# Kernel tuning notes

Hardware: AMD Instinct MI355X
Metric: run time of the kernel (lower is better)

Reference implementation:

```python
import jax, jax.numpy as jnp
import numpy as np

D_MODEL = 1024
D_K = 1024
D_V = 1024
THRESH = 0.9
LN_EPS = 1e-6


def setup_inputs() -> dict:
    key = jax.random.key(0)
    ks = jax.random.split(key, 8)
    B, S = 8, 2048
    scale = 1.0 / np.sqrt(D_MODEL)
    return {
        "q": jax.random.normal(ks[0], (B, S, D_MODEL), dtype=jnp.float32),
        "k": jax.random.normal(ks[1], (B, S, D_MODEL), dtype=jnp.float32),
        "v": jax.random.normal(ks[2], (B, S, D_MODEL), dtype=jnp.float32),
        "Wq": jax.random.normal(ks[3], (D_MODEL, D_K), dtype=jnp.float32) * scale,
        "Wk": jax.random.normal(ks[4], (D_MODEL, D_K), dtype=jnp.float32) * scale,
        "Wv": jax.random.normal(ks[5], (D_MODEL, D_V), dtype=jnp.float32) * scale,
        "Wfc": jax.random.normal(ks[6], (D_V, D_MODEL), dtype=jnp.float32) * (1.0 / np.sqrt(D_V)),
        "ln_gamma": jnp.ones((D_MODEL,), dtype=jnp.float32),
        "ln_beta": jnp.zeros((D_MODEL,), dtype=jnp.float32),
    }


def reference(q, k, v, Wq, Wk, Wv, Wfc, ln_gamma, ln_beta):
    residual = q
    qh = q @ Wq          # [B,S,d_k]
    kh = k @ Wk          # [B,S,d_k]
    vh = v @ Wv          # [B,S,d_v]
    inv_sqrt_dk = jnp.asarray(1.0 / np.sqrt(D_K), dtype=qh.dtype)
    attn = jnp.einsum('bqd,bkd->bqk', qh, kh) * inv_sqrt_dk  # [B,S,S]
    # hard sparsity threshold applied BEFORE softmax (faithful to original)
    attn = jnp.where(attn < THRESH, jnp.asarray(0.0, attn.dtype), attn)
    attn = jax.nn.softmax(attn, axis=-1)
    # dropout is identity in eval mode
    out = jnp.einsum('bqk,bkd->bqd', attn, vh) @ Wfc  # [B,S,d_model]
    out = out + residual
    mean = jnp.mean(out, axis=-1, keepdims=True)
    var = jnp.mean(jnp.square(out - mean), axis=-1, keepdims=True)
    out = (out - mean) * jax.lax.rsqrt(var + LN_EPS) * ln_gamma + ln_beta
    return (out, attn)
```

## Files before the change

kernel.cpp:

```cpp
#include <hip/hip_runtime.h>
#include <hip/hip_bf16.h>
#include <stdint.h>

typedef __attribute__((ext_vector_type(8))) short bf16x8;
typedef __attribute__((ext_vector_type(4))) float f32x4;
typedef __attribute__((ext_vector_type(4))) unsigned short us4;
typedef __attribute__((ext_vector_type(8))) unsigned short us8;

__device__ __forceinline__ unsigned short f2bf(float f) {
  union { float f; unsigned int u; } v; v.f = f;
  unsigned int u = v.u;
  return (unsigned short)((u + 0x7FFFu + ((u >> 16) & 1u)) >> 16);
}
__device__ __forceinline__ float bf2f(unsigned short h) {
  union { unsigned int u; float f; } v; v.u = ((unsigned int)h) << 16;
  return v.f;
}

__device__ __forceinline__ void gload16(const unsigned short* g, unsigned short* l) {
  __builtin_amdgcn_global_load_lds(
      (const __attribute__((address_space(1))) unsigned int*)g,
      (__attribute__((address_space(3))) unsigned int*)l, 16, 0, 0);
}

template <int EPI>
__global__ __launch_bounds__(512, 2)
void gemm2p(const unsigned short* __restrict__ Ap, const unsigned short* __restrict__ Btp,
            void* __restrict__ Cp, float* __restrict__ extra,
            int M, int N, int K, int nbm, int nbn,
            long long sA, long long sB, long long sC)
{
  __shared__ unsigned short ls[65536];
  __shared__ float srow[256][4];

  const int tid = threadIdx.x;
  const int lane = tid & 63;
  const int wid = tid >> 6;
  const int bb = blockIdx.y;
  const int bm = blockIdx.x % nbm, bn = blockIdx.x / nbm;
  const int row0 = bm * 256, col0 = bn * 256;

  const unsigned short* Ab = Ap + (long long)bb * sA;
  const unsigned short* Bb = Btp + (long long)bb * sB;

  const int srw = tid >> 3;
  const int ssl = (tid & 7) ^ ((tid >> 3) & 7);
  const unsigned short* Asrc = Ab + (long long)(row0 + srw) * K + ssl * 8;
  const unsigned short* Bsrc = Bb + (long long)(col0 + srw) * K + ssl * 8;

#define STAGE(KT, BUF) do { \
    unsigned short* _la = ls + (BUF) * 32768 + wid * 512; \
    unsigned short* _lb = _la + 16384; \
    const long long _ko = (long long)(KT) * 64; \
    gload16(Asrc + _ko,             _la); \
    gload16(Asrc + 64ll * K + _ko,  _la + 4096); \
    gload16(Asrc + 128ll * K + _ko, _la + 8192); \
    gload16(Asrc + 192ll * K + _ko, _la + 12288); \
    gload16(Bsrc + _ko,             _lb); \
    gload16(Bsrc + 64ll * K + _ko,  _lb + 4096); \
    gload16(Bsrc + 128ll * K + _ko, _lb + 8192); \
    gload16(Bsrc + 192ll * K + _ko, _lb + 12288); \
  } while (0)

  const int arow = (wid >> 2) * 128 + (lane & 15);
  const int bcol = (wid & 3) * 64 + (lane & 15);
  const int sl0 = ((lane >> 4) ^ (lane & 7)) * 8;
  const int sl1 = ((4 + (lane >> 4)) ^ (lane & 7)) * 8;

  f32x4 acc[8][4];
#pragma unroll
  for (int m = 0; m < 8; ++m)
#pragma unroll
    for (int n = 0; n < 4; ++n) {
      f32x4 z = {0.f, 0.f, 0.f, 0.f};
      acc[m][n] = z;
    }

  STAGE(0, 0);
  const int NT = K >> 6;
  for (int t = 0; t < NT; ++t) {
    const int cb = (t & 1) * 32768;
    asm volatile("s_waitcnt vmcnt(0)" ::: "memory");
    __builtin_amdgcn_s_barrier();
    __builtin_amdgcn_sched_barrier(0);
    if (t + 1 < NT) STAGE(t + 1, (t & 1) ^ 1);
    const unsigned short* As = ls + cb;
    const unsigned short* Bs = ls + cb + 16384;
    bf16x8 af[8], bfr[4];
#pragma unroll
    for (int mf = 0; mf < 8; ++mf)
      af[mf] = *(const bf16x8*)&As[(arow + mf * 16) * 64 + sl0];
#pragma unroll
    for (int nf = 0; nf < 4; ++nf)
      bfr[nf] = *(const bf16x8*)&Bs[(bcol + nf * 16) * 64 + sl0];
    __builtin_amdgcn_s_setprio(1);
#pragma unroll
    for (int mf = 0; mf < 8; ++mf)
#pragma unroll
      for (int nf = 0; nf < 4; ++nf)
        acc[mf][nf] = __builtin_amdgcn_mfma_f32_16x16x32_bf16(af[mf], bfr[nf], acc[mf][nf], 0, 0, 0);
    __builtin_amdgcn_s_setprio(0);
#pragma unroll
    for (int mf = 0; mf < 8; ++mf)
      af[mf] = *(const bf16x8*)&As[(arow + mf * 16) * 64 + sl1];
#pragma unroll
    for (int nf = 0; nf < 4; ++nf)
      bfr[nf] = *(const bf16x8*)&Bs[(bcol + nf * 16) * 64 + sl1];
    __builtin_amdgcn_s_setprio(1);
#pragma unroll
    for (int mf = 0; mf < 8; ++mf)
#pragma unroll
      for (int nf = 0; nf < 4; ++nf)
        acc[mf][nf] = __builtin_amdgcn_mfma_f32_16x16x32_bf16(af[mf], bfr[nf], acc[mf][nf], 0, 0, 0);
    __builtin_amdgcn_s_setprio(0);
  }
#undef STAGE

  if (EPI == 0 || EPI == 3) {
    unsigned short* C = (unsigned short*)Cp + (long long)bb * sC;
    const float* inv = (EPI == 3) ? (extra + (long long)bb * 2048) : nullptr;
#pragma unroll
    for (int mf = 0; mf < 8; ++mf)
#pragma unroll
      for (int nf = 0; nf < 4; ++nf)
#pragma unroll
        for (int i = 0; i < 4; ++i) {
          int gr = row0 + (wid >> 2) * 128 + mf * 16 + (lane >> 4) * 4 + i;
          int gc = col0 + (wid & 3) * 64 + nf * 16 + (lane & 15);
          float x = acc[mf][nf][i];
          if (EPI == 3) x *= inv[gr];
          C[(long long)gr * N + gc] = f2bf(x);
        }
  } else if (EPI == 2) {
    unsigned short* C = (unsigned short*)Cp;
#pragma unroll
    for (int mf = 0; mf < 8; ++mf)
#pragma unroll
      for (int nf = 0; nf < 4; ++nf) {
        int gr = row0 + (wid >> 2) * 128 + mf * 16 + (lane >> 4) * 4;
        int gc = col0 + (wid & 3) * 64 + nf * 16 + (lane & 15);
        int bb2 = gr >> 11, grb = gr & 2047;
        us4 o;
        o[0] = f2bf(acc[mf][nf][0]); o[1] = f2bf(acc[mf][nf][1]);
        o[2] = f2bf(acc[mf][nf][2]); o[3] = f2bf(acc[mf][nf][3]);
        *(us4*)&C[(long long)bb2 * sC + (long long)gc * 2048 + grb] = o;
      }
  } else {
    unsigned short* C = (unsigned short*)Cp + (long long)bb * sC;
    float rs[8][4];
#pragma unroll
    for (int mf = 0; mf < 8; ++mf)
#pragma unroll
      for (int i = 0; i < 4; ++i) rs[mf][i] = 0.f;
#pragma unroll
    for (int mf = 0; mf < 8; ++mf)
#pragma unroll
      for (int nf = 0; nf < 4; ++nf)
#pragma unroll
        for (int i = 0; i < 4; ++i) {
          int gr = row0 + (wid >> 2) * 128 + mf * 16 + (lane >> 4) * 4 + i;
          int gc = col0 + (wid & 3) * 64 + nf * 16 + (lane & 15);
          float s = acc[mf][nf][i] * 0.03125f;
          s = (s < 0.9f) ? 0.f : s;
          float e = __expf(s);
          C[(long long)gr * N + gc] = f2bf(e);
          rs[mf][i] += e;
        }
#pragma unroll
    for (int mf = 0; mf < 8; ++mf)
#pragma unroll
      for (int i = 0; i < 4; ++i) {
        float vv = rs[mf][i];
        vv += __shfl_xor(vv, 1); vv += __shfl_xor(vv, 2);
        vv += __shfl_xor(vv, 4); vv += __shfl_xor(vv, 8);
        if ((lane & 15) == 0)
          srow[(wid >> 2) * 128 + mf * 16 + (lane >> 4) * 4 + i][wid & 3] = vv;
      }
    __syncthreads();
    if (tid < 256) {
      int gr = row0 + tid;
      extra[((long long)bb * M + gr) * nbn + bn] =
          srow[tid][0] + srow[tid][1] + srow[tid][2] + srow[tid][3];
    }
  }
}

__global__ __launch_bounds__(256)
void cvt3(const float* __restrict__ a, const float* __restrict__ b,
          const float* __restrict__ c, unsigned short* __restrict__ oa,
          unsigned short* __restrict__ ob, unsigned short* __restrict__ oc) {
  const long long i = ((long long)blockIdx.x * 256 + threadIdx.x) * 8;
#pragma unroll
  for (int p = 0; p < 3; ++p) {
    const float* src = (p == 0) ? a : (p == 1) ? b : c;
    unsigned short* dst = (p == 0) ? oa : (p == 1) ? ob : oc;
    f32x4 x0 = *(const f32x4*)(src + i);
    f32x4 x1 = *(const f32x4*)(src + i + 4);
    us8 o;
    o[0] = f2bf(x0[0]); o[1] = f2bf(x0[1]); o[2] = f2bf(x0[2]); o[3] = f2bf(x0[3]);
    o[4] = f2bf(x1[0]); o[5] = f2bf(x1[1]); o[6] = f2bf(x1[2]); o[7] = f2bf(x1[3]);
    *(us8*)(dst + i) = o;
  }
}

__global__ __launch_bounds__(256)
void wtrans4(const float* __restrict__ W0, const float* __restrict__ W1,
             const float* __restrict__ W2, const float* __restrict__ W3,
             unsigned short* __restrict__ T0, unsigned short* __restrict__ T1,
             unsigned short* __restrict__ T2, unsigned short* __restrict__ T3) {
  __shared__ float t[32][33];
  const int z = blockIdx.z;
  const float* W = (z == 0) ? W0 : (z == 1) ? W1 : (z == 2) ? W2 : W3;
  unsigned short* WT = (z == 0) ? T0 : (z == 1) ? T1 : (z == 2) ? T2 : T3;
  const int bi = blockIdx.x, bj = blockIdx.y;
  const int c = threadIdx.x & 31;
  const int r0 = threadIdx.x >> 5;
#pragma unroll
  for (int j = 0; j < 4; ++j) {
    int r = r0 + j * 8;
    t[r][c] = W[(long long)(bi * 32 + r) * 1024 + bj * 32 + c];
  }
  __syncthreads();
#pragma unroll
  for (int j = 0; j < 4; ++j) {
    int r = r0 + j * 8;
    WT[(long long)(bj * 32 + r) * 1024 + bi * 32 + c] = f2bf(t[c][r]);
  }
}

__global__ __launch_bounds__(256)
void attn_norm(const unsigned short* __restrict__ e, const float* __restrict__ partials,
               float* __restrict__ attn, float* __restrict__ inv_dens) {
  const long long row = blockIdx.x;
  const int tid = threadIdx.x;
  __shared__ float sden;
  if (tid < 64) {
    float v = (tid < 8) ? partials[row * 8 + tid] : 0.f;
    v += __shfl_xor(v, 1); v += __shfl_xor(v, 2); v += __shfl_xor(v, 4);
    if (tid == 0) sden = v;
  }
  __syncthreads();
  const float inv = 1.0f / sden;
  if (tid == 0) inv_dens[row] = inv;
  us8 x = *(const us8*)(e + row * 2048 + tid * 8);
  f32x4 y0, y1;
#pragma unroll
  for (int i = 0; i < 4; ++i) { y0[i] = bf2f(x[i]) * inv; y1[i] = bf2f(x[i + 4]) * inv; }
  *(f32x4*)(attn + row * 2048 + tid * 8) = y0;
  *(f32x4*)(attn + row * 2048 + tid * 8 + 4) = y1;
}

template <bool QB16>
__global__ __launch_bounds__(256)
void ln_kernel(const unsigned short* __restrict__ fc, const void* __restrict__ qres,
               const float* __restrict__ gamma, const float* __restrict__ beta,
               float* __restrict__ out) {
  const long long row = blockIdx.x;
  const int tid = threadIdx.x;
  __shared__ float sb1[4], sb2[4];
  us4 hv = *(const us4*)(fc + row * 1024 + tid * 4);
  float q0, q1, q2, q3;
  if (QB16) {
    us4 qv = *(const us4*)((const unsigned short*)qres + row * 1024 + tid * 4);
    q0 = bf2f(qv[0]); q1 = bf2f(qv[1]); q2 = bf2f(qv[2]); q3 = bf2f(qv[3]);
  } else {
    f32x4 qv = *(const f32x4*)((const float*)qres + row * 1024 + tid * 4);
    q0 = qv[0]; q1 = qv[1]; q2 = qv[2]; q3 = qv[3];
  }
  float x0 = bf2f(hv[0]) + q0;
  float x1 = bf2f(hv[1]) + q1;
  float x2 = bf2f(hv[2]) + q2;
  float x3 = bf2f(hv[3]) + q3;
  float s = x0 + x1 + x2 + x3;
#pragma unroll
  for (int m = 1; m < 64; m <<= 1) s += __shfl_xor(s, m);
  if ((tid & 63) == 0) sb1[tid >> 6] = s;
  __syncthreads();
  const float mean = (sb1[0] + sb1[1] + sb1[2] + sb1[3]) * (1.0f / 1024.0f);
  float d0 = x0 - mean, d1 = x1 - mean, d2 = x2 - mean, d3 = x3 - mean;
  float vs = d0 * d0 + d1 * d1 + d2 * d2 + d3 * d3;
#pragma unroll
  for (int m = 1; m < 64; m <<= 1) vs += __shfl_xor(vs, m);
  if ((tid & 63) == 0) sb2[tid >> 6] = vs;
  __syncthreads();
  const float var = (sb2[0] + sb2[1] + sb2[2] + sb2[3]) * (1.0f / 1024.0f);
  const float r = rsqrtf(var + 1e-6f);
  f32x4 g = *(const f32x4*)(gamma + tid * 4);
  f32x4 bt = *(const f32x4*)(beta + tid * 4);
  f32x4 o;
  o[0] = d0 * r * g[0] + bt[0];
  o[1] = d1 * r * g[1] + bt[1];
  o[2] = d2 * r * g[2] + bt[2];
  o[3] = d3 * r * g[3] + bt[3];
  *(f32x4*)(out + row * 1024 + tid * 4) = o;
}

extern "C" void kernel_launch(void* const* d_in, const int* in_sizes, int n_in,
                              void* d_out, int out_size, void* d_ws, size_t ws_size,
                              hipStream_t stream) {
  const float* q    = (const float*)d_in[0];
  const float* k    = (const float*)d_in[1];
  const float* v    = (const float*)d_in[2];
  const float* Wq   = (const float*)d_in[3];
  const float* Wk   = (const float*)d_in[4];
  const float* Wv   = (const float*)d_in[5];
  const float* Wfc  = (const float*)d_in[6];
  const float* gamma = (const float*)d_in[7];
  const float* beta  = (const float*)d_in[8];

  float* out0 = (float*)d_out;
  float* attn = out0 + (long long)8 * 2048 * 1024;

  char* ao = (char*)attn;
  unsigned short* kb = (unsigned short*)(ao + (32ll << 20));
  unsigned short* vb = (unsigned short*)(ao + (64ll << 20));
  unsigned short* qh = (unsigned short*)(ao + (96ll << 20));
  unsigned short* kh = (unsigned short*)(ao);
  unsigned short* vhT     = (unsigned short*)d_out;
  unsigned short* out_mid = (unsigned short*)((char*)d_out + (32ll << 20));

  char* ws = (char*)d_ws;
  unsigned short* WqT  = (unsigned short*)(ws);
  unsigned short* WkT  = (unsigned short*)(ws + (2ll  << 20));
  unsigned short* WvT  = (unsigned short*)(ws + (4ll  << 20));
  unsigned short* WfcT = (unsigned short*)(ws + (6ll  << 20));
  float* partials      = (float*)(ws + (8ll  << 20));
  float* inv_dens      = (float*)(ws + (10ll << 20));
  unsigned short* e    = (unsigned short*)(ws + (11ll << 20));
  unsigned short* fc   = e;
  const bool qb_ws = ws_size >= (110ll << 20);
  unsigned short* qb = qb_ws ? (unsigned short*)(ws + (76ll << 20))
                             : (unsigned short*)(ao);

  cvt3<<<dim3(8192), 256, 0, stream>>>(q, k, v, qb, kb, vb);
  wtrans4<<<dim3(32, 32, 4), 256, 0, stream>>>(Wq, Wk, Wv, Wfc, WqT, WkT, WvT, WfcT);

  gemm2p<0><<<dim3(256, 1), 512, 0, stream>>>(qb, WqT, qh, nullptr,
      16384, 1024, 1024, 64, 4, 0, 0, 0);
  gemm2p<0><<<dim3(256, 1), 512, 0, stream>>>(kb, WkT, kh, nullptr,
      16384, 1024, 1024, 64, 4, 0, 0, 0);
  gemm2p<2><<<dim3(256, 1), 512, 0, stream>>>(vb, WvT, vhT, nullptr,
      16384, 1024, 1024, 64, 4, 0, 0, 1024ll * 2048);

  gemm2p<1><<<dim3(64, 8), 512, 0, stream>>>(qh, kh, e, partials,
      2048, 2048, 1024, 8, 8, 2048ll * 1024, 2048ll * 1024, 2048ll * 2048);

  attn_norm<<<dim3(16384), 256, 0, stream>>>(e, partials, attn, inv_dens);

  gemm2p<3><<<dim3(32, 8), 512, 0, stream>>>(e, vhT, out_mid, inv_dens,
      2048, 1024, 2048, 8, 4, 2048ll * 2048, 1024ll * 2048, 2048ll * 1024);

  gemm2p<0><<<dim3(256, 1), 512, 0, stream>>>(out_mid, WfcT, fc, nullptr,
      16384, 1024, 1024, 64, 4, 0, 0, 0);

  if (qb_ws)
    ln_kernel<true><<<dim3(16384), 256, 0, stream>>>(fc, qb, gamma, beta, out0);
  else
    ln_kernel<false><<<dim3(16384), 256, 0, stream>>>(fc, q, gamma, beta, out0);
}
```

Baseline: 411.6 us.

## Use smaller 128x128 tile GEMM kernel for QK^T score computation

```diff
diff --git a/kernel.cpp b/kernel.cpp
--- a/kernel.cpp
+++ b/kernel.cpp
@@ -21,6 +21,124 @@
   __builtin_amdgcn_global_load_lds(
       (const __attribute__((address_space(1))) unsigned int*)g,
       (__attribute__((address_space(3))) unsigned int*)l, 16, 0, 0);
+}
+
+template <int EPI>
+__global__ __launch_bounds__(256, 2)
+void gemm_nt(const unsigned short* __restrict__ Ap, const unsigned short* __restrict__ Btp,
+             void* __restrict__ Cp, float* __restrict__ extra,
+             int M, int N, int K, int nbm,
+             long long sA, long long sB, long long sC)
+{
+  const int tid = threadIdx.x;
+  const int lane = tid & 63;
+  const int wid = tid >> 6;
+  const int wr = wid >> 1, wc = wid & 1;
+  const int bb = blockIdx.y;
+  const int bm = blockIdx.x % nbm, bn = blockIdx.x / nbm;
+  const int row0 = bm * 128, col0 = bn * 128;
+
+  __shared__ unsigned short lsA[128 * 64];
+  __shared__ unsigned short lsB[128 * 64];
+  __shared__ float srow2[128][2];
+
+  const unsigned short* Ab = Ap + (long long)bb * sA;
+  const unsigned short* Bb = Btp + (long long)bb * sB;
+
+  const int srow = wid * 32 + (lane >> 3);
+  const int sslot = (lane & 7) ^ (lane >> 3);
+  const unsigned short* Asrc = Ab + (long long)(row0 + srow) * K + sslot * 8;
+  const unsigned short* Bsrc = Bb + (long long)(col0 + srow) * K + sslot * 8;
+  unsigned short* ldsA0 = &lsA[wid * 2048];
+  unsigned short* ldsB0 = &lsB[wid * 2048];
+
+  f32x4 acc[4][4];
+#pragma unroll
+  for (int i = 0; i < 4; ++i)
+#pragma unroll
+    for (int j = 0; j < 4; ++j) {
+      f32x4 z = {0.f, 0.f, 0.f, 0.f};
+      acc[i][j] = z;
+    }
+
+  for (int k0 = 0; k0 < K; k0 += 64) {
+    __syncthreads();
+#pragma unroll
+    for (int it = 0; it < 4; ++it) {
+      gload16(Asrc + (long long)it * 8 * K + k0, ldsA0 + it * 512);
+      gload16(Bsrc + (long long)it * 8 * K + k0, ldsB0 + it * 512);
+    }
+    __syncthreads();
+#pragma unroll
+    for (int kk = 0; kk < 2; ++kk) {
+      int kslot = kk * 4 + (lane >> 4);
+      bf16x8 af[4], bfg[4];
+#pragma unroll
+      for (int mf = 0; mf < 4; ++mf) {
+        int rl = wr * 64 + mf * 16 + (lane & 15);
+        af[mf] = *(const bf16x8*)&lsA[rl * 64 + ((kslot ^ (rl & 7)) * 8)];
+      }
+#pragma unroll
+      for (int nf = 0; nf < 4; ++nf) {
+        int cl = wc * 64 + nf * 16 + (lane & 15);
+        bfg[nf] = *(const bf16x8*)&lsB[cl * 64 + ((kslot ^ (cl & 7)) * 8)];
+      }
+#pragma unroll
+      for (int mf = 0; mf < 4; ++mf)
+#pragma unroll
+        for (int nf = 0; nf < 4; ++nf)
+          acc[mf][nf] = __builtin_amdgcn_mfma_f32_16x16x32_bf16(af[mf], bfg[nf], acc[mf][nf], 0, 0, 0);
+    }
+  }
+
+  unsigned short* C = (unsigned short*)Cp + (long long)bb * sC;
+  if (EPI == 0) {
+#pragma unroll
+    for (int mf = 0; mf < 4; ++mf)
+#pragma unroll
+      for (int nf = 0; nf < 4; ++nf)
+#pragma unroll
+        for (int i = 0; i < 4; ++i) {
+          int gr = row0 + wr * 64 + mf * 16 + (lane >> 4) * 4 + i;
+          int gc = col0 + wc * 64 + nf * 16 + (lane & 15);
+          C[(long long)gr * N + gc] = f2bf(acc[mf][nf][i]);
+        }
+  } else {
+    float rs[4][4];
+#pragma unroll
+    for (int mf = 0; mf < 4; ++mf)
+#pragma unroll
+      for (int i = 0; i < 4; ++i) rs[mf][i] = 0.f;
+#pragma unroll
+    for (int mf = 0; mf < 4; ++mf)
+#pragma unroll
+      for (int nf = 0; nf < 4; ++nf)
+#pragma unroll
+        for (int i = 0; i < 4; ++i) {
+          int gr = row0 + wr * 64 + mf * 16 + (lane >> 4) * 4 + i;
+          int gc = col0 + wc * 64 + nf * 16 + (lane & 15);
+          float s = acc[mf][nf][i] * 0.03125f;
+          s = (s < 0.9f) ? 0.f : s;
+          float e = __expf(s);
+          C[(long long)gr * N + gc] = f2bf(e);
+          rs[mf][i] += e;
+        }
+#pragma unroll
+    for (int mf = 0; mf < 4; ++mf)
+#pragma unroll
+      for (int i = 0; i < 4; ++i) {
+        float vv = rs[mf][i];
+        vv += __shfl_xor(vv, 1); vv += __shfl_xor(vv, 2);
+        vv += __shfl_xor(vv, 4); vv += __shfl_xor(vv, 8);
+        if ((lane & 15) == 0)
+          srow2[wr * 64 + mf * 16 + (lane >> 4) * 4 + i][wc] = vv;
+      }
+    __syncthreads();
+    if (tid < 128) {
+      int gr = row0 + tid;
+      extra[((long long)bb * M + gr) * 16 + bn] = srow2[tid][0] + srow2[tid][1];
+    }
+  }
 }
 
 template <int EPI>
@@ -31,7 +149,6 @@
             long long sA, long long sB, long long sC)
 {
   __shared__ unsigned short ls[65536];
-  __shared__ float srow[256][4];
 
   const int tid = threadIdx.x;
   const int lane = tid & 63;
@@ -145,43 +262,6 @@
         o[2] = f2bf(acc[mf][nf][2]); o[3] = f2bf(acc[mf][nf][3]);
         *(us4*)&C[(long long)bb2 * sC + (long long)gc * 2048 + grb] = o;
       }
-  } else {
-    unsigned short* C = (unsigned short*)Cp + (long long)bb * sC;
-    float rs[8][4];
-#pragma unroll
-    for (int mf = 0; mf < 8; ++mf)
-#pragma unroll
-      for (int i = 0; i < 4; ++i) rs[mf][i] = 0.f;
-#pragma unroll
-    for (int mf = 0; mf < 8; ++mf)
-#pragma unroll
-      for (int nf = 0; nf < 4; ++nf)
-#pragma unroll
-        for (int i = 0; i < 4; ++i) {
-          int gr = row0 + (wid >> 2) * 128 + mf * 16 + (lane >> 4) * 4 + i;
-          int gc = col0 + (wid & 3) * 64 + nf * 16 + (lane & 15);
-          float s = acc[mf][nf][i] * 0.03125f;
-          s = (s < 0.9f) ? 0.f : s;
-          float e = __expf(s);
-          C[(long long)gr * N + gc] = f2bf(e);
-          rs[mf][i] += e;
-        }
-#pragma unroll
-    for (int mf = 0; mf < 8; ++mf)
-#pragma unroll
-      for (int i = 0; i < 4; ++i) {
-        float vv = rs[mf][i];
-        vv += __shfl_xor(vv, 1); vv += __shfl_xor(vv, 2);
-        vv += __shfl_xor(vv, 4); vv += __shfl_xor(vv, 8);
-        if ((lane & 15) == 0)
-          srow[(wid >> 2) * 128 + mf * 16 + (lane >> 4) * 4 + i][wid & 3] = vv;
-      }
-    __syncthreads();
-    if (tid < 256) {
-      int gr = row0 + tid;
-      extra[((long long)bb * M + gr) * nbn + bn] =
-          srow[tid][0] + srow[tid][1] + srow[tid][2] + srow[tid][3];
-    }
   }
 }
 
@@ -235,8 +315,9 @@
   const int tid = threadIdx.x;
   __shared__ float sden;
   if (tid < 64) {
-    float v = (tid < 8) ? partials[row * 8 + tid] : 0.f;
-    v += __shfl_xor(v, 1); v += __shfl_xor(v, 2); v += __shfl_xor(v, 4);
+    float v = (tid < 16) ? partials[row * 16 + tid] : 0.f;
+    v += __shfl_xor(v, 1); v += __shfl_xor(v, 2);
+    v += __shfl_xor(v, 4); v += __shfl_xor(v, 8);
     if (tid == 0) sden = v;
   }
   __syncthreads();
@@ -342,8 +423,8 @@
   gemm2p<2><<<dim3(256, 1), 512, 0, stream>>>(vb, WvT, vhT, nullptr,
       16384, 1024, 1024, 64, 4, 0, 0, 1024ll * 2048);
 
-  gemm2p<1><<<dim3(64, 8), 512, 0, stream>>>(qh, kh, e, partials,
-      2048, 2048, 1024, 8, 8, 2048ll * 1024, 2048ll * 1024, 2048ll * 2048);
+  gemm_nt<1><<<dim3(256, 8), 256, 0, stream>>>(qh, kh, e, partials,
+      2048, 2048, 1024, 16, 2048ll * 1024, 2048ll * 1024, 2048ll * 2048);
 
   attn_norm<<<dim3(16384), 256, 0, stream>>>(e, partials, attn, inv_dens);
 
```

After: 404.4 us. No clear change (-1.7%).
